# Kernel tuning notes

Measured on AMD Instinct MI355X. Metric: run time of the kernel, lower is better.

The kernel has to match this reference:

```python
import jax, jax.numpy as jnp
import numpy as np

C = 1.0            # curvature args.c
EPS = 1e-7         # Hyperboloid eps for float32
MIN_NORM = 1e-15
MAX_SQDIST = 50.0
NUM_LAYERS = 3     # args.num_layers (resSumGCN hops)
MARGIN = 0.1       # args.margin
N_NODES = 200000
NUM_USERS = 100000
EMB_DIM = 64
E_ADJ = 1600000
E_TR = 65536
NUM_NEG = 16


def _mink_dot(x, y, keepdim=True):
    # Minkowski inner product: -x0*y0 + sum_i xi*yi
    res = jnp.sum(x * y, axis=-1) - 2.0 * x[..., 0] * y[..., 0]
    return res[..., None] if keepdim else res


def _sqdist(x, y, c):
    K = 1.0 / c
    prod = _mink_dot(x, y)                      # [E, 1]
    theta = jnp.maximum(-prod / K, 1.0 + EPS)
    return jnp.minimum(K * jnp.arccosh(theta) ** 2, MAX_SQDIST)


def _expmap0(u, c):
    sqrtK = (1.0 / c) ** 0.5
    x = u[..., 1:]
    x_norm = jnp.maximum(jnp.linalg.norm(x, axis=-1, keepdims=True), MIN_NORM)
    theta = x_norm / sqrtK
    first = sqrtK * jnp.cosh(theta)
    rest = sqrtK * jnp.sinh(theta) * x / x_norm
    return jnp.concatenate([first, rest], axis=-1)


def _logmap0(x, c):
    sqrtK = (1.0 / c) ** 0.5
    y = x[..., 1:]
    y_norm = jnp.maximum(jnp.linalg.norm(y, axis=-1, keepdims=True), MIN_NORM)
    theta = jnp.maximum(x[..., :1] / sqrtK, 1.0 + EPS)
    rest = sqrtK * jnp.arccosh(theta) * y / y_norm
    return jnp.concatenate([jnp.zeros_like(rest[..., :1]), rest], axis=-1)


def _proj(x, c):
    K = 1.0 / c
    y = x[..., 1:]
    first = jnp.sqrt(K + jnp.sum(y * y, axis=-1, keepdims=True))
    return jnp.concatenate([first, y], axis=-1)


def setup_inputs() -> dict:
    key = jax.random.key(0)
    ks = jax.random.split(key, 8)
    # embedding init: uniform(-scale, scale) tangent vector, then expmap0 onto hyperboloid
    tan = jax.random.uniform(ks[0], (N_NODES, EMB_DIM), minval=-0.1, maxval=0.1, dtype=jnp.float32)
    weight = _expmap0(tan, C)
    adj_row = jnp.sort(jax.random.randint(ks[1], (E_ADJ,), 0, N_NODES, dtype=jnp.int32))
    adj_col = jax.random.randint(ks[2], (E_ADJ,), 0, N_NODES, dtype=jnp.int32)
    # mimic symmetric-normalized adjacency values (~1/deg)
    adj_vals = jax.random.uniform(ks[3], (E_ADJ,), dtype=jnp.float32) * 0.125
    anchor = jax.random.randint(ks[4], (E_TR,), 0, NUM_USERS, dtype=jnp.int32)
    pos = jax.random.randint(ks[5], (E_TR,), 0, NUM_USERS, dtype=jnp.int32) + NUM_USERS
    neg = jax.random.randint(ks[6], (E_TR, NUM_NEG), 0, NUM_USERS, dtype=jnp.int32) + NUM_USERS
    return {"weight": weight, "adj_vals": adj_vals, "adj_row": adj_row,
            "adj_col": adj_col, "anchor": anchor, "pos": pos, "neg": neg}


def _encode(weight, adj_row, adj_col, adj_vals):
    # HypAgg: logmap0 -> resSumGCN (sum of adj^k x for k=1..L) -> expmap0 -> proj
    x_t = _logmap0(weight, C)
    h = x_t
    acc = jnp.zeros_like(x_t)
    for _ in range(NUM_LAYERS):
        h = jax.ops.segment_sum(adj_vals[:, None] * h[adj_col], adj_row,
                                num_segments=N_NODES, indices_are_sorted=True)
        acc = acc + h
    return _proj(_expmap0(acc, C), C)


def reference(weight, adj_vals, adj_row, adj_col, anchor, pos, neg):
    h = _encode(weight, adj_row, adj_col, adj_vals)      # [N, d] on hyperboloid
    emb_a = h[anchor]                                    # [E, d]
    emb_p = h[pos]                                       # [E, d]
    # decode_pos: sqdist + hratio weight
    pos_scores = _sqdist(emb_a, emb_p, C)                # [E, 1]
    u0 = emb_a[:, 0]
    i0 = emb_p[:, 0]
    score = (1.0 - _mink_dot(emb_a, emb_p, keepdim=False) - u0 - i0) / (u0 * i0)
    w = jax.nn.sigmoid(-score)[:, None]                  # [E, 1]
    # decode_neg: hard-negative mining (euclidean sqdist to positive, take min)
    d2 = jnp.sum((h[neg] - emb_p[:, None, :]) ** 2, axis=-1)   # [E, num_neg]
    hard_idx = jnp.argmin(d2, axis=1)
    hard_neg = jnp.take_along_axis(neg, hard_idx[:, None], axis=1)[:, 0]
    neg_scores = _sqdist(emb_a, h[hard_neg], C)          # [E, 1]
    # margin ranking loss with hyperbolic-ratio weight
    loss = jnp.sum(jnp.maximum(pos_scores - neg_scores + MARGIN * w, 0.0))
    return loss
```

## Files before the change

kernel.cpp:

```cpp
#include <hip/hip_runtime.h>
#include <hip/hip_bf16.h>
#include <math.h>

#define N_NODES 200000
#define EMB_DIM 64
#define E_ADJ 1600000
#define E_TR 65536
#define NUM_NEG 16
#define EPS 1e-7f
#define MIN_NORM 1e-15f
#define MAX_SQDIST 50.0f
#define MARGIN 0.1f
#define LOSS_BLOCKS (E_TR / 4)
#define SPMM_BLOCKS 2048
#define NWAVES (SPMM_BLOCKS * 4)
#define RPW 25
#define LDS_CAP 512

#define PACK_BLOCKS ((E_ADJ + 255) / 256)
#define RP_BLOCKS   ((N_NODES + 1 + 255) / 256)
#define LOG_BLOCKS  ((N_NODES + 15) / 16)

typedef float f4 __attribute__((ext_vector_type(4)));

__device__ __forceinline__ float group_reduce16(float v) {
    v += __shfl_xor(v, 8, 64);
    v += __shfl_xor(v, 4, 64);
    v += __shfl_xor(v, 2, 64);
    v += __shfl_xor(v, 1, 64);
    return v;
}

__device__ __forceinline__ float dot4(f4 a, f4 b) {
    return a.x * b.x + a.y * b.y + a.z * b.z + a.w * b.w;
}

__device__ __forceinline__ unsigned bfr(float f) {
    unsigned u = __float_as_uint(f);
    return (u + 0x7fffu + ((u >> 16) & 1u)) >> 16;
}
__device__ __forceinline__ uint2 f42bf(f4 v) {
    return make_uint2(bfr(v.x) | (bfr(v.y) << 16), bfr(v.z) | (bfr(v.w) << 16));
}
__device__ __forceinline__ f4 bf2f4(uint2 g) {
    f4 r;
    r.x = __uint_as_float(g.x << 16);
    r.y = __uint_as_float(g.x & 0xffff0000u);
    r.z = __uint_as_float(g.y << 16);
    r.w = __uint_as_float(g.y & 0xffff0000u);
    return r;
}

__global__ void prelude_kernel(const int* __restrict__ cols, const float* __restrict__ vals,
                               int2* __restrict__ ev, const int* __restrict__ rows,
                               int* __restrict__ rp, const float* __restrict__ w,
                               uint2* __restrict__ xt) {
    int b = blockIdx.x;
    if (b < PACK_BLOCKS) {
        int i = b * 256 + threadIdx.x;
        if (i < E_ADJ) ev[i] = make_int2(cols[i] << 4, __float_as_int(vals[i]));
    } else if (b < PACK_BLOCKS + RP_BLOCKS) {
        int r = (b - PACK_BLOCKS) * 256 + threadIdx.x;
        if (r <= N_NODES) {
            int lo = 0, hi = E_ADJ;
            while (lo < hi) {
                int mid = (lo + hi) >> 1;
                if (rows[mid] < r) lo = mid + 1; else hi = mid;
            }
            rp[r] = lo;
        }
    } else {
        int bb = b - PACK_BLOCKS - RP_BLOCKS;
        int wave = bb * 4 + (threadIdx.x >> 6);
        int lane = threadIdx.x & 63;
        int e = lane >> 4, d = lane & 15;
        int node = wave * 4 + e;
        if (node < N_NODES) {
            f4 v = ((const f4*)w)[(node << 4) + d];
            f4 y = v;
            if (d == 0) y.x = 0.0f;
            float n2 = group_reduce16(dot4(y, y));
            float ynorm = fmaxf(sqrtf(n2), MIN_NORM);
            float w0 = __shfl(v.x, lane & 48, 64);
            float theta = fmaxf(w0, 1.0f + EPS);
            float scale = acoshf(theta) / ynorm;
            xt[(node << 4) + d] = f42bf(y * scale);
        }
    }
}

__device__ __forceinline__ f4 row_accum(const uint2* __restrict__ h_in,
                                        const int2* __restrict__ ev,
                                        const int2* L, int ebase, int staged,
                                        int s, int e, int d) {
    f4 acc = {0.f, 0.f, 0.f, 0.f};
    int k = s;
    for (; k + 2 <= e; k += 2) {
        int o0 = k - ebase;
        int2 cv0, cv1;
        if (o0 + 1 < staged) { cv0 = L[o0]; cv1 = L[o0 + 1]; }
        else                 { cv0 = ev[k]; cv1 = ev[k + 1]; }
        uint2 g0 = h_in[cv0.x + d];
        uint2 g1 = h_in[cv1.x + d];
        acc += bf2f4(g0) * __int_as_float(cv0.y);
        acc += bf2f4(g1) * __int_as_float(cv1.y);
    }
    if (k < e) {
        int o = k - ebase;
        int2 cv;
        if (o < staged) cv = L[o]; else cv = ev[k];
        uint2 gg = h_in[cv.x + d];
        acc += bf2f4(gg) * __int_as_float(cv.y);
    }
    return acc;
}

__global__ __launch_bounds__(256) void spmm_kernel(const uint2* __restrict__ h_in,
                                                   uint2* __restrict__ h_out,
                                                   const int2* __restrict__ ev,
                                                   const int* __restrict__ rp) {
    __shared__ int2 evs[4][LDS_CAP];
    int wib = threadIdx.x >> 6;
    int lane = threadIdx.x & 63;
    int g = lane >> 4, d = lane & 15;
    int wid = __builtin_amdgcn_readfirstlane(blockIdx.x * 4 + wib);
    int r0 = wid * RPW;
    if (r0 >= N_NODES) return;
    int r1 = min(r0 + RPW, N_NODES);
    int ebase = rp[r0];
    int etot  = rp[r1];
    int staged = min(etot - ebase, LDS_CAP);
    int2* L = evs[wib];
    for (int k = lane; k < staged; k += 64)
        L[k] = ev[ebase + k];
    __syncthreads();

    for (int base = r0; base < r1; base += 4) {
        int row = base + g;
        bool valid = row < r1;
        int s = 0, e = 0;
        if (valid) { s = rp[row]; e = rp[row + 1]; }
        f4 acc = row_accum(h_in, ev, L, ebase, staged, s, e, d);
        if (valid)
            h_out[(row << 4) + d] = f42bf(acc);
    }
}

__global__ __launch_bounds__(256) void spmm_expmap_kernel(const uint2* __restrict__ h_gather,
                                                          const uint2* __restrict__ h1,
                                                          const uint2* __restrict__ h2,
                                                          float* __restrict__ h,
                                                          float* __restrict__ nrm2,
                                                          const int2* __restrict__ ev,
                                                          const int* __restrict__ rp) {
    __shared__ int2 evs[4][LDS_CAP];
    int wib = threadIdx.x >> 6;
    int lane = threadIdx.x & 63;
    int g = lane >> 4, d = lane & 15;
    int wid = __builtin_amdgcn_readfirstlane(blockIdx.x * 4 + wib);
    int r0 = wid * RPW;
    if (r0 >= N_NODES) return;
    int r1 = min(r0 + RPW, N_NODES);
    int ebase = rp[r0];
    int etot  = rp[r1];
    int staged = min(etot - ebase, LDS_CAP);
    int2* L = evs[wib];
    for (int k = lane; k < staged; k += 64)
        L[k] = ev[ebase + k];
    __syncthreads();

    for (int base = r0; base < r1; base += 4) {
        int row = base + g;
        bool valid = row < r1;
        int s = 0, e = 0;
        int oi = (row << 4) + d;
        f4 a1 = {0.f,0.f,0.f,0.f}, a2 = {0.f,0.f,0.f,0.f};
        if (valid) {
            s = rp[row]; e = rp[row + 1];
            a1 = bf2f4(h1[oi]);
            a2 = bf2f4(h2[oi]);
        }
        f4 acc = row_accum(h_gather, ev, L, ebase, staged, s, e, d);
        if (valid) {
            f4 u = (a1 + a2) + acc;
            f4 x = u;
            if (d == 0) x.x = 0.0f;
            float n2 = group_reduce16(dot4(x, x));
            float xn = fmaxf(sqrtf(n2), MIN_NORM);
            float sh = sinhf(xn);
            f4 rest = x * (sh / xn);
            float r2 = group_reduce16(dot4(rest, rest));
            float first = sqrtf(1.0f + r2);
            f4 ov = rest;
            if (d == 0) ov.x = first;
            ((f4*)h)[oi] = ov;
            if (d == 0) nrm2[row] = first * first + r2;
        }
    }
}

__global__ void loss_kernel(const float* __restrict__ h, const float* __restrict__ nrm2,
                            const int* __restrict__ anchor, const int* __restrict__ pos,
                            const int* __restrict__ neg, float* __restrict__ partials) {
    int wib = threadIdx.x >> 6;
    int lane = threadIdx.x & 63;
    int e = lane >> 4, d = lane & 15;
    int i = __builtin_amdgcn_readfirstlane(blockIdx.x * 4 + wib);
    const f4* H = (const f4*)h;

    int ia = anchor[i], ip = pos[i];
    f4 a4 = H[(ia << 4) + d];
    f4 p4 = H[(ip << 4) + d];
    int4 nb4 = ((const int4*)(neg + (size_t)i * NUM_NEG))[e];

    float s[4];
    s[0] = dot4(p4, H[(nb4.x << 4) + d]);
    s[1] = dot4(p4, H[(nb4.y << 4) + d]);
    s[2] = dot4(p4, H[(nb4.z << 4) + d]);
    s[3] = dot4(p4, H[(nb4.w << 4) + d]);
    float dap = dot4(a4, p4);

    {
        bool hi = (d & 8) != 0;
        float send0 = hi ? s[0] : s[2];
        float send1 = hi ? s[1] : s[3];
        float r0 = __shfl_xor(send0, 8, 64);
        float r1 = __shfl_xor(send1, 8, 64);
        float k0 = hi ? s[2] : s[0];
        float k1 = hi ? s[3] : s[1];
        s[0] = k0 + r0;
        s[1] = k1 + r1;
    }
    float sv;
    {
        bool hi = (d & 4) != 0;
        float send = hi ? s[0] : s[1];
        float r = __shfl_xor(send, 4, 64);
        float k = hi ? s[1] : s[0];
        sv = k + r;
    }
    sv += __shfl_xor(sv, 2, 64);
    sv += __shfl_xor(sv, 1, 64);
    int b_lane = ((d >> 3) & 1) * 2 + ((d >> 2) & 1);
    int nidx_lane = (d & 8) ? ((d & 4) ? nb4.w : nb4.z)
                            : ((d & 4) ? nb4.y : nb4.x);
    int j_lane = 4 * e + b_lane;

    float np2 = nrm2[ip];
    float bd = nrm2[nidx_lane] + np2 - 2.0f * sv;
    int bj = j_lane;
    #pragma unroll
    for (int off = 32; off > 0; off >>= 1) {
        float od = __shfl_xor(bd, off, 64);
        int   oj = __shfl_xor(bj, off, 64);
        if (od < bd || (od == bd && oj < bj)) { bd = od; bj = oj; }
    }
    int bn = neg[(size_t)i * NUM_NEG + __builtin_amdgcn_readfirstlane(bj)];
    f4 w4 = H[(bn << 4) + d];
    float dan = group_reduce16(dot4(a4, w4));
    dap = group_reduce16(dap);

    float loss = 0.0f;
    if (lane == 0) {
        float a0 = a4.x, p0 = p4.x, n0 = w4.x;
        float mink = dap - 2.0f * a0 * p0;
        float th = fmaxf(-mink, 1.0f + EPS);
        float ac = acoshf(th);
        float pos_score = fminf(ac * ac, MAX_SQDIST);
        float score = (1.0f - mink - a0 - p0) / (a0 * p0);
        float wgt = 1.0f / (1.0f + expf(score));
        float minkn = dan - 2.0f * a0 * n0;
        float thn = fmaxf(-minkn, 1.0f + EPS);
        float acn = acoshf(thn);
        float neg_score = fminf(acn * acn, MAX_SQDIST);
        loss = fmaxf(pos_score - neg_score + MARGIN * wgt, 0.0f);
    }
    __shared__ float part[4];
    if (lane == 0) part[wib] = loss;
    __syncthreads();
    if (threadIdx.x == 0)
        partials[blockIdx.x] = part[0] + part[1] + part[2] + part[3];
}

__global__ void reduce_kernel(const float* __restrict__ partials, float* __restrict__ out) {
    int tid = threadIdx.x;
    float s = 0.0f;
    for (int i = tid; i < LOSS_BLOCKS; i += 1024)
        s += partials[i];
    #pragma unroll
    for (int off = 32; off > 0; off >>= 1)
        s += __shfl_xor(s, off, 64);
    __shared__ float part[16];
    if ((tid & 63) == 0) part[tid >> 6] = s;
    __syncthreads();
    if (tid == 0) {
        float t = 0.0f;
        #pragma unroll
        for (int k = 0; k < 16; ++k) t += part[k];
        out[0] = t;
    }
}

extern "C" void kernel_launch(void* const* d_in, const int* in_sizes, int n_in,
                              void* d_out, int out_size, void* d_ws, size_t ws_size,
                              hipStream_t stream) {
    const float* weight   = (const float*)d_in[0];
    const float* adj_vals = (const float*)d_in[1];
    const int*   adj_row  = (const int*)d_in[2];
    const int*   adj_col  = (const int*)d_in[3];
    const int*   anchor   = (const int*)d_in[4];
    const int*   pos      = (const int*)d_in[5];
    const int*   neg      = (const int*)d_in[6];
    float* out = (float*)d_out;

    const size_t NODEF32 = (size_t)N_NODES * EMB_DIM * sizeof(float);
    const size_t NODEBF  = (size_t)N_NODES * EMB_DIM * sizeof(unsigned short);
    const size_t MB = 1024 * 1024;
    char* ws = (char*)d_ws;
    float* hfin = (float*)(ws);
    uint2* bf0  = (uint2*)(ws + NODEF32);
    uint2* bf1  = (uint2*)(ws + NODEF32 + NODEBF);
    uint2* bf2  = (uint2*)(ws + NODEF32 + 2 * NODEBF);
    int*   rp   = (int*)  (ws + NODEF32 + 3 * NODEBF);
    float* nrm2 = (float*)(ws + NODEF32 + 3 * NODEBF + 1 * MB);
    int2*  ev   = (int2*) (ws + NODEF32 + 3 * NODEBF + 2 * MB);
    float* partials = (float*)(ws + NODEF32 + 3 * NODEBF + 16 * MB);

    prelude_kernel<<<PACK_BLOCKS + RP_BLOCKS + LOG_BLOCKS, 256, 0, stream>>>(
        adj_col, adj_vals, ev, adj_row, rp, weight, bf0);
    spmm_kernel<<<SPMM_BLOCKS, 256, 0, stream>>>(bf0, bf1, ev, rp);
    spmm_kernel<<<SPMM_BLOCKS, 256, 0, stream>>>(bf1, bf2, ev, rp);
    spmm_expmap_kernel<<<SPMM_BLOCKS, 256, 0, stream>>>(bf2, bf1, bf2, hfin, nrm2, ev, rp);
    loss_kernel<<<LOSS_BLOCKS, 256, 0, stream>>>(hfin, nrm2, anchor, pos, neg, partials);
    reduce_kernel<<<1, 1024, 0, stream>>>(partials, out);
}
```

Before: 332.2 us.

## Gather bf16 rows with 16-byte loads using 8 lanes per row in SpMM

Each SpMM row is now handled by 8 lanes with uint4 (8 bf16) loads instead of 16 lanes with uint2 loads, so a wave processes 8 rows per iteration. Column indices are pre-shifted by 3 to match the new stride. The per-edge LDS-versus-global branch is replaced by one wave-uniform choice: LDS when the whole edge range fits, global otherwise. The goal is fewer, wider gather instructions and more rows in flight, at the cost of more registers per lane and smaller reductions in the expmap epilogue.

```diff
diff --git a/kernel.cpp b/kernel.cpp
--- a/kernel.cpp
+++ b/kernel.cpp
@@ -31,6 +31,13 @@
     return v;
 }
 
+__device__ __forceinline__ float group_reduce8(float v) {
+    v += __shfl_xor(v, 4, 64);
+    v += __shfl_xor(v, 2, 64);
+    v += __shfl_xor(v, 1, 64);
+    return v;
+}
+
 __device__ __forceinline__ float dot4(f4 a, f4 b) {
     return a.x * b.x + a.y * b.y + a.z * b.z + a.w * b.w;
 }
@@ -51,6 +58,20 @@
     return r;
 }
 
+__device__ __forceinline__ void fma8(f4& a0, f4& a1, uint4 g, float v) {
+    f4 lo, hi;
+    lo.x = __uint_as_float(g.x << 16);
+    lo.y = __uint_as_float(g.x & 0xffff0000u);
+    lo.z = __uint_as_float(g.y << 16);
+    lo.w = __uint_as_float(g.y & 0xffff0000u);
+    hi.x = __uint_as_float(g.z << 16);
+    hi.y = __uint_as_float(g.z & 0xffff0000u);
+    hi.z = __uint_as_float(g.w << 16);
+    hi.w = __uint_as_float(g.w & 0xffff0000u);
+    a0 += lo * v;
+    a1 += hi * v;
+}
+
 __global__ void prelude_kernel(const int* __restrict__ cols, const float* __restrict__ vals,
                                int2* __restrict__ ev, const int* __restrict__ rows,
                                int* __restrict__ rp, const float* __restrict__ w,
@@ -58,7 +79,7 @@
     int b = blockIdx.x;
     if (b < PACK_BLOCKS) {
         int i = b * 256 + threadIdx.x;
-        if (i < E_ADJ) ev[i] = make_int2(cols[i] << 4, __float_as_int(vals[i]));
+        if (i < E_ADJ) ev[i] = make_int2(cols[i] << 3, __float_as_int(vals[i]));
     } else if (b < PACK_BLOCKS + RP_BLOCKS) {
         int r = (b - PACK_BLOCKS) * 256 + threadIdx.x;
         if (r <= N_NODES) {
@@ -89,66 +110,83 @@
     }
 }
 
-__device__ __forceinline__ f4 row_accum(const uint2* __restrict__ h_in,
-                                        const int2* __restrict__ ev,
-                                        const int2* L, int ebase, int staged,
-                                        int s, int e, int d) {
-    f4 acc = {0.f, 0.f, 0.f, 0.f};
+__device__ __forceinline__ void row_accum_lds(f4& a0, f4& a1,
+                                              const uint4* __restrict__ h_in,
+                                              const int2* L, int s, int e, int d) {
     int k = s;
     for (; k + 2 <= e; k += 2) {
-        int o0 = k - ebase;
-        int2 cv0, cv1;
-        if (o0 + 1 < staged) { cv0 = L[o0]; cv1 = L[o0 + 1]; }
-        else                 { cv0 = ev[k]; cv1 = ev[k + 1]; }
-        uint2 g0 = h_in[cv0.x + d];
-        uint2 g1 = h_in[cv1.x + d];
-        acc += bf2f4(g0) * __int_as_float(cv0.y);
-        acc += bf2f4(g1) * __int_as_float(cv1.y);
+        int2 cv0 = L[k];
+        int2 cv1 = L[k + 1];
+        uint4 g0 = h_in[cv0.x + d];
+        uint4 g1 = h_in[cv1.x + d];
+        fma8(a0, a1, g0, __int_as_float(cv0.y));
+        fma8(a0, a1, g1, __int_as_float(cv1.y));
     }
     if (k < e) {
-        int o = k - ebase;
-        int2 cv;
-        if (o < staged) cv = L[o]; else cv = ev[k];
-        uint2 gg = h_in[cv.x + d];
-        acc += bf2f4(gg) * __int_as_float(cv.y);
-    }
-    return acc;
-}
-
-__global__ __launch_bounds__(256) void spmm_kernel(const uint2* __restrict__ h_in,
-                                                   uint2* __restrict__ h_out,
+        int2 cv = L[k];
+        fma8(a0, a1, h_in[cv.x + d], __int_as_float(cv.y));
+    }
+}
+
+__device__ __forceinline__ void row_accum_glb(f4& a0, f4& a1,
+                                              const uint4* __restrict__ h_in,
+                                              const int2* __restrict__ ev,
+                                              int s, int e, int d) {
+    int k = s;
+    for (; k + 2 <= e; k += 2) {
+        int2 cv0 = ev[k];
+        int2 cv1 = ev[k + 1];
+        uint4 g0 = h_in[cv0.x + d];
+        uint4 g1 = h_in[cv1.x + d];
+        fma8(a0, a1, g0, __int_as_float(cv0.y));
+        fma8(a0, a1, g1, __int_as_float(cv1.y));
+    }
+    if (k < e) {
+        int2 cv = ev[k];
+        fma8(a0, a1, h_in[cv.x + d], __int_as_float(cv.y));
+    }
+}
+
+__global__ __launch_bounds__(256) void spmm_kernel(const uint4* __restrict__ h_in,
+                                                   uint4* __restrict__ h_out,
                                                    const int2* __restrict__ ev,
                                                    const int* __restrict__ rp) {
     __shared__ int2 evs[4][LDS_CAP];
     int wib = threadIdx.x >> 6;
     int lane = threadIdx.x & 63;
-    int g = lane >> 4, d = lane & 15;
+    int g = lane >> 3, d = lane & 7;
     int wid = __builtin_amdgcn_readfirstlane(blockIdx.x * 4 + wib);
     int r0 = wid * RPW;
     if (r0 >= N_NODES) return;
     int r1 = min(r0 + RPW, N_NODES);
     int ebase = rp[r0];
     int etot  = rp[r1];
-    int staged = min(etot - ebase, LDS_CAP);
+    int nst   = etot - ebase;
+    bool allst = nst <= LDS_CAP;
+    int staged = min(nst, LDS_CAP);
     int2* L = evs[wib];
     for (int k = lane; k < staged; k += 64)
         L[k] = ev[ebase + k];
     __syncthreads();
 
-    for (int base = r0; base < r1; base += 4) {
+    for (int base = r0; base < r1; base += 8) {
         int row = base + g;
         bool valid = row < r1;
         int s = 0, e = 0;
         if (valid) { s = rp[row]; e = rp[row + 1]; }
-        f4 acc = row_accum(h_in, ev, L, ebase, staged, s, e, d);
-        if (valid)
-            h_out[(row << 4) + d] = f42bf(acc);
-    }
-}
-
-__global__ __launch_bounds__(256) void spmm_expmap_kernel(const uint2* __restrict__ h_gather,
-                                                          const uint2* __restrict__ h1,
-                                                          const uint2* __restrict__ h2,
+        f4 a0 = {0.f, 0.f, 0.f, 0.f}, a1 = {0.f, 0.f, 0.f, 0.f};
+        if (allst) row_accum_lds(a0, a1, h_in, L, s - ebase, e - ebase, d);
+        else       row_accum_glb(a0, a1, h_in, ev, s, e, d);
+        if (valid) {
+            uint2 p0 = f42bf(a0), p1 = f42bf(a1);
+            h_out[(row << 3) + d] = make_uint4(p0.x, p0.y, p1.x, p1.y);
+        }
+    }
+}
+
+__global__ __launch_bounds__(256) void spmm_expmap_kernel(const uint4* __restrict__ h_gather,
+                                                          const uint4* __restrict__ h1,
+                                                          const uint4* __restrict__ h2,
                                                           float* __restrict__ h,
                                                           float* __restrict__ nrm2,
                                                           const int2* __restrict__ ev,
@@ -156,45 +194,53 @@
     __shared__ int2 evs[4][LDS_CAP];
     int wib = threadIdx.x >> 6;
     int lane = threadIdx.x & 63;
-    int g = lane >> 4, d = lane & 15;
+    int g = lane >> 3, d = lane & 7;
     int wid = __builtin_amdgcn_readfirstlane(blockIdx.x * 4 + wib);
     int r0 = wid * RPW;
     if (r0 >= N_NODES) return;
     int r1 = min(r0 + RPW, N_NODES);
     int ebase = rp[r0];
     int etot  = rp[r1];
-    int staged = min(etot - ebase, LDS_CAP);
+    int nst   = etot - ebase;
+    bool allst = nst <= LDS_CAP;
+    int staged = min(nst, LDS_CAP);
     int2* L = evs[wib];
     for (int k = lane; k < staged; k += 64)
         L[k] = ev[ebase + k];
     __syncthreads();
 
-    for (int base = r0; base < r1; base += 4) {
+    for (int base = r0; base < r1; base += 8) {
         int row = base + g;
         bool valid = row < r1;
         int s = 0, e = 0;
-        int oi = (row << 4) + d;
-        f4 a1 = {0.f,0.f,0.f,0.f}, a2 = {0.f,0.f,0.f,0.f};
+        uint4 b1 = make_uint4(0, 0, 0, 0), b2 = make_uint4(0, 0, 0, 0);
         if (valid) {
             s = rp[row]; e = rp[row + 1];
-            a1 = bf2f4(h1[oi]);
-            a2 = bf2f4(h2[oi]);
-        }
-        f4 acc = row_accum(h_gather, ev, L, ebase, staged, s, e, d);
+            b1 = h1[(row << 3) + d];
+            b2 = h2[(row << 3) + d];
+        }
+        f4 a0 = {0.f, 0.f, 0.f, 0.f}, a1 = {0.f, 0.f, 0.f, 0.f};
+        if (allst) row_accum_lds(a0, a1, h_gather, L, s - ebase, e - ebase, d);
+        else       row_accum_glb(a0, a1, h_gather, ev, s, e, d);
         if (valid) {
-            f4 u = (a1 + a2) + acc;
-            f4 x = u;
-            if (d == 0) x.x = 0.0f;
-            float n2 = group_reduce16(dot4(x, x));
+            f4 h1lo = bf2f4(make_uint2(b1.x, b1.y)), h1hi = bf2f4(make_uint2(b1.z, b1.w));
+            f4 h2lo = bf2f4(make_uint2(b2.x, b2.y)), h2hi = bf2f4(make_uint2(b2.z, b2.w));
+            f4 u0 = (h1lo + h2lo) + a0;
+            f4 u1 = (h1hi + h2hi) + a1;
+            f4 x0 = u0, x1 = u1;
+            if (d == 0) x0.x = 0.0f;
+            float n2 = group_reduce8(dot4(x0, x0) + dot4(x1, x1));
             float xn = fmaxf(sqrtf(n2), MIN_NORM);
             float sh = sinhf(xn);
-            f4 rest = x * (sh / xn);
-            float r2 = group_reduce16(dot4(rest, rest));
-            float first = sqrtf(1.0f + r2);
-            f4 ov = rest;
-            if (d == 0) ov.x = first;
-            ((f4*)h)[oi] = ov;
-            if (d == 0) nrm2[row] = first * first + r2;
+            float sc = sh / xn;
+            f4 rv0 = x0 * sc, rv1 = x1 * sc;
+            float rr2 = group_reduce8(dot4(rv0, rv0) + dot4(rv1, rv1));
+            float first = sqrtf(1.0f + rr2);
+            f4 o0 = rv0, o1 = rv1;
+            if (d == 0) o0.x = first;
+            ((f4*)h)[(row << 4) + 2 * d]     = o0;
+            ((f4*)h)[(row << 4) + 2 * d + 1] = o1;
+            if (d == 0) nrm2[row] = first * first + rr2;
         }
     }
 }
@@ -319,8 +365,8 @@
     char* ws = (char*)d_ws;
     float* hfin = (float*)(ws);
     uint2* bf0  = (uint2*)(ws + NODEF32);
-    uint2* bf1  = (uint2*)(ws + NODEF32 + NODEBF);
-    uint2* bf2  = (uint2*)(ws + NODEF32 + 2 * NODEBF);
+    char*  bf1  = (char*) (ws + NODEF32 + NODEBF);
+    char*  bf2  = (char*) (ws + NODEF32 + 2 * NODEBF);
     int*   rp   = (int*)  (ws + NODEF32 + 3 * NODEBF);
     float* nrm2 = (float*)(ws + NODEF32 + 3 * NODEBF + 1 * MB);
     int2*  ev   = (int2*) (ws + NODEF32 + 3 * NODEBF + 2 * MB);
@@ -328,9 +374,10 @@
 
     prelude_kernel<<<PACK_BLOCKS + RP_BLOCKS + LOG_BLOCKS, 256, 0, stream>>>(
         adj_col, adj_vals, ev, adj_row, rp, weight, bf0);
-    spmm_kernel<<<SPMM_BLOCKS, 256, 0, stream>>>(bf0, bf1, ev, rp);
-    spmm_kernel<<<SPMM_BLOCKS, 256, 0, stream>>>(bf1, bf2, ev, rp);
-    spmm_expmap_kernel<<<SPMM_BLOCKS, 256, 0, stream>>>(bf2, bf1, bf2, hfin, nrm2, ev, rp);
+    spmm_kernel<<<SPMM_BLOCKS, 256, 0, stream>>>((const uint4*)bf0, (uint4*)bf1, ev, rp);
+    spmm_kernel<<<SPMM_BLOCKS, 256, 0, stream>>>((const uint4*)bf1, (uint4*)bf2, ev, rp);
+    spmm_expmap_kernel<<<SPMM_BLOCKS, 256, 0, stream>>>((const uint4*)bf2, (const uint4*)bf1,
+                                                        (const uint4*)bf2, hfin, nrm2, ev, rp);
     loss_kernel<<<LOSS_BLOCKS, 256, 0, stream>>>(hfin, nrm2, anchor, pos, neg, partials);
     reduce_kernel<<<1, 1024, 0, stream>>>(partials, out);
 }
```

Result: faster. 305.5 us (-8.0%).
